# Kernel tuning notes

Hardware: AMD Instinct MI355X
Metric: run time of the kernel (lower is better)

## Reference

```python
import jax, jax.numpy as jnp
import numpy as np

B, S, D = 4, 2048, 512
DT_RANK, N = 32, 16  # dt_rank, d_state
EPS = 1e-5


def setup_inputs() -> dict:
    key = jax.random.key(0)
    ks = jax.random.split(key, 8)
    def w(k, shape, scale):
        return jax.random.normal(k, shape, dtype=jnp.float32) * scale
    return {
        "x": w(ks[0], (B, S, D), 1.0),
        "gamma": jnp.ones((D,), jnp.float32),
        "beta": jnp.zeros((D,), jnp.float32),
        "W_proj": w(ks[1], (D, D), D ** -0.5),
        "b_proj": jnp.zeros((D,), jnp.float32),
        "W_fwd": w(ks[2], (D, D), D ** -0.5),
        "b_fwd": jnp.zeros((D,), jnp.float32),
        "W_bwd": w(ks[3], (D, D), D ** -0.5),
        "b_bwd": jnp.zeros((D,), jnp.float32),
        "W_dbc": w(ks[4], (D, DT_RANK + 2 * N), D ** -0.5),
        "W_dt": w(ks[5], (DT_RANK, D), DT_RANK ** -0.5),
        "b_dt": jnp.zeros((D,), jnp.float32),
        "A_log": jnp.log(jnp.tile(jnp.arange(1, N + 1, dtype=jnp.float32), (D, 1))),
        "D_ssm": jnp.ones((D,), jnp.float32),
    }


def _ssm(x, A_log, D_ssm, W_dbc, W_dt, b_dt):
    # x: (B, S, D) with D == dim_inner
    A = -jnp.exp(A_log)                                   # (D, N)
    dbc = x @ W_dbc                                       # (B, S, dt_rank + 2N)
    delta = jax.nn.softplus(dbc[..., :DT_RANK] @ W_dt + b_dt)  # (B, S, D)
    Bm = dbc[..., DT_RANK:DT_RANK + N]                    # (B, S, N)
    Cm = dbc[..., DT_RANK + N:]                           # (B, S, N)
    deltaA = jnp.exp(delta[..., None] * A)                # (B, S, D, N)
    BX = (delta * x)[..., None] * Bm[:, :, None, :]       # (B, S, D, N)
    def combine(c1, c2):
        a1, b1 = c1
        a2, b2 = c2
        return a1 * a2, a2 * b1 + b2
    _, hs = jax.lax.associative_scan(combine, (deltaA, BX), axis=1)
    y = jnp.einsum('bsdn,bsn->bsd', hs, Cm) + D_ssm * x
    return y


def reference(x, gamma, beta, W_proj, b_proj, W_fwd, b_fwd, W_bwd, b_bwd,
              W_dbc, W_dt, b_dt, A_log, D_ssm):
    skip = x
    mu = jnp.mean(x, axis=-1, keepdims=True)
    var = jnp.var(x, axis=-1, keepdims=True)
    xn = (x - mu) * jax.lax.rsqrt(var + EPS) * gamma + beta
    z1 = xn @ W_proj + b_proj
    x1 = z1  # source applies the SAME self.proj twice -> identical outputs
    # kernel-size-1 conv1d == pointwise linear over channels
    fwd = x1 @ W_fwd + b_fwd
    x1_ssm = _ssm(fwd, A_log, D_ssm, W_dbc, W_dt, b_dt)  # computed but unused in source (dead code)
    bwd = x1 @ W_bwd + bb if False else x1 @ W_bwd + b_bwd
    x2 = _ssm(bwd, A_log, D_ssm, W_dbc, W_dt, b_dt)
    z = jax.nn.silu(z1)
    return x1 * z + x2 * z + skip
```

## Files before the change

kernel.cpp:

```cpp
#include <hip/hip_runtime.h>
#include <hip/hip_bf16.h>
#include <math.h>

#define Bb 4
#define Sdim 2048
#define Ddim 512
#define Nn16 16
#define TOK 8192
#define NCh 64
#define LCh 32

using bf16x8 = __attribute__((ext_vector_type(8))) __bf16;
using f32x4  = __attribute__((ext_vector_type(4))) float;

__device__ __forceinline__ unsigned short f2bf(float f) {
    unsigned int u = __float_as_uint(f);
    u += 0x7fffu + ((u >> 16) & 1u);
    return (unsigned short)(u >> 16);
}
__device__ __forceinline__ float bf2f(unsigned short h) {
    return __uint_as_float(((unsigned int)h) << 16);
}

#define GLD16(g, l) __builtin_amdgcn_global_load_lds( \
    (const __attribute__((address_space(1))) void*)(g), \
    (__attribute__((address_space(3))) void*)(l), 16, 0, 0)

__device__ __forceinline__ float softplus_f(float v) {
    return v > 20.f ? v : log1pf(__expf(v));
}

__global__ __launch_bounds__(256) void prep_all(
    const float* __restrict__ x, const float* __restrict__ gamma, const float* __restrict__ beta,
    const float* __restrict__ Wp, const float* __restrict__ Wb,
    const float* __restrict__ Wdbc, const float* __restrict__ Wdt,
    ushort* __restrict__ xn, ushort* __restrict__ Wpt, ushort* __restrict__ Wbt,
    ushort* __restrict__ Wdbct, ushort* __restrict__ WdtT)
{
    int blk = blockIdx.x;
    int tid = threadIdx.x;
    if (blk < 560) {
        __shared__ float tb[32 * 33];
        int xx = tid & 31, yy0 = tid >> 5;
        const float* in; ushort* outT; int K, N, bx, by;
        if (blk < 256)      { in = Wp;   outT = Wpt;   K = 512; N = 512; bx = (blk & 15) * 32; by = (blk >> 4) * 32; }
        else if (blk < 512) { int t = blk - 256; in = Wb; outT = Wbt; K = 512; N = 512; bx = (t & 15) * 32; by = (t >> 4) * 32; }
        else if (blk < 544) { int t = blk - 512; in = Wdbc; outT = Wdbct; K = 512; N = 64; bx = (t & 1) * 32; by = (t >> 1) * 32; }
        else                { int t = blk - 544; in = Wdt; outT = WdtT; K = 32; N = 512; bx = t * 32; by = 0; }
        #pragma unroll
        for (int yy = yy0; yy < 32; yy += 8)
            tb[yy * 33 + xx] = in[(size_t)(by + yy) * N + bx + xx];
        __syncthreads();
        #pragma unroll
        for (int yy = yy0; yy < 32; yy += 8)
            outT[(size_t)(bx + yy) * K + by + xx] = f2bf(tb[xx * 33 + yy]);
    } else {
        int bid = blk - 560;
        int w = tid >> 6, lane = tid & 63;
        const float4* g4 = (const float4*)gamma;
        const float4* b4 = (const float4*)beta;
        float4 g0 = g4[lane], g1 = g4[lane + 64];
        float4 be0 = b4[lane], be1 = b4[lane + 64];
        for (int rr = 0; rr < 8; ++rr) {
            int row = bid * 32 + w * 8 + rr;
            const float4* xr = (const float4*)(x + (size_t)row * Ddim);
            float4 v0 = xr[lane];
            float4 v1 = xr[lane + 64];
            float s = v0.x + v0.y + v0.z + v0.w + v1.x + v1.y + v1.z + v1.w;
            float q = v0.x*v0.x + v0.y*v0.y + v0.z*v0.z + v0.w*v0.w
                    + v1.x*v1.x + v1.y*v1.y + v1.z*v1.z + v1.w*v1.w;
            #pragma unroll
            for (int m = 1; m <= 32; m <<= 1) { s += __shfl_xor(s, m); q += __shfl_xor(q, m); }
            float mu = s * (1.0f / Ddim);
            float var = q * (1.0f / Ddim) - mu * mu;
            float rs = rsqrtf(var + 1e-5f);
            ushort4 u0, u1;
            u0.x = f2bf((v0.x - mu) * rs * g0.x + be0.x);
            u0.y = f2bf((v0.y - mu) * rs * g0.y + be0.y);
            u0.z = f2bf((v0.z - mu) * rs * g0.z + be0.z);
            u0.w = f2bf((v0.w - mu) * rs * g0.w + be0.w);
            u1.x = f2bf((v1.x - mu) * rs * g1.x + be1.x);
            u1.y = f2bf((v1.y - mu) * rs * g1.y + be1.y);
            u1.z = f2bf((v1.z - mu) * rs * g1.z + be1.z);
            u1.w = f2bf((v1.w - mu) * rs * g1.w + be1.w);
            *(ushort4*)(xn + (size_t)row * Ddim + lane * 4) = u0;
            *(ushort4*)(xn + (size_t)row * Ddim + 256 + lane * 4) = u1;
        }
    }
}

__global__ __launch_bounds__(256) void gemm64(
    const ushort* __restrict__ A,
    const ushort* __restrict__ Bt,
    const float* __restrict__ bias,
    ushort* __restrict__ Cb)
{
    __shared__ __align__(16) ushort As[64 * 64];
    __shared__ __align__(16) ushort Bs[64 * 64];
    int tid = threadIdx.x, w = tid >> 6, lane = tid & 63;
    int bm = blockIdx.x * 64, bn = blockIdx.y * 64;
    int quad = lane >> 4, l16 = lane & 15;
    int srow8 = lane >> 3;
    int scolx = ((lane & 7) ^ srow8) * 8;
    int cof0 = (quad ^ (l16 & 7)) * 8;
    int cof1 = ((4 + quad) ^ (l16 & 7)) * 8;
    f32x4 acc[4] = {};

    for (int k0 = 0; k0 < 512; k0 += 64) {
        __syncthreads();
        #pragma unroll
        for (int s = 0; s < 2; ++s) {
            int r = w * 16 + s * 8;
            GLD16(A  + (size_t)(bm + r + srow8) * 512 + k0 + scolx, &As[r * 64]);
            GLD16(Bt + (size_t)(bn + r + srow8) * 512 + k0 + scolx, &Bs[r * 64]);
        }
        __syncthreads();
        #pragma unroll
        for (int ks = 0; ks < 2; ++ks) {
            int cof = ks ? cof1 : cof0;
            bf16x8 bfr = *(const bf16x8*)(const void*)&Bs[(w * 16 + l16) * 64 + cof];
            #pragma unroll
            for (int i = 0; i < 4; ++i) {
                bf16x8 af = *(const bf16x8*)(const void*)&As[(16 * i + l16) * 64 + cof];
                acc[i] = __builtin_amdgcn_mfma_f32_16x16x32_bf16(af, bfr, acc[i], 0, 0, 0);
            }
        }
    }
    int col = bn + w * 16 + l16;
    float bv = bias[col];
    #pragma unroll
    for (int i = 0; i < 4; ++i) {
        int row = bm + 16 * i + quad * 4;
        #pragma unroll
        for (int r = 0; r < 4; ++r)
            Cb[(size_t)(row + r) * 512 + col] = f2bf(acc[i][r] + bv);
    }
}

__global__ __launch_bounds__(256) void dbc_delta(
    const ushort* __restrict__ bwd,
    const ushort* __restrict__ Wdbct,
    const ushort* __restrict__ WdtT,
    const float* __restrict__ b_dt,
    float* __restrict__ BC,
    ushort* __restrict__ delta)
{
    __shared__ __align__(16) ushort As[32 * 64];
    __shared__ __align__(16) ushort Bs[64 * 64];
    __shared__ __align__(16) ushort sdbc[32 * 32];
    int tid = threadIdx.x, w = tid >> 6, lane = tid & 63;
    int bm = blockIdx.x * 32;
    int quad = lane >> 4, l16 = lane & 15;
    int srow8 = lane >> 3;
    int scolx = ((lane & 7) ^ srow8) * 8;
    int cof0 = (quad ^ (l16 & 7)) * 8;
    int cof1 = ((4 + quad) ^ (l16 & 7)) * 8;

    f32x4 acc[2] = {};
    for (int k0 = 0; k0 < 512; k0 += 64) {
        __syncthreads();
        {
            int r = w * 8;
            GLD16(bwd + (size_t)(bm + r + srow8) * 512 + k0 + scolx, &As[r * 64]);
        }
        #pragma unroll
        for (int s = 0; s < 2; ++s) {
            int r = w * 16 + s * 8;
            GLD16(Wdbct + (size_t)(r + srow8) * 512 + k0 + scolx, &Bs[r * 64]);
        }
        __syncthreads();
        #pragma unroll
        for (int ks = 0; ks < 2; ++ks) {
            int cof = ks ? cof1 : cof0;
            bf16x8 bfr = *(const bf16x8*)(const void*)&Bs[(w * 16 + l16) * 64 + cof];
            #pragma unroll
            for (int i = 0; i < 2; ++i) {
                bf16x8 af = *(const bf16x8*)(const void*)&As[(16 * i + l16) * 64 + cof];
                acc[i] = __builtin_amdgcn_mfma_f32_16x16x32_bf16(af, bfr, acc[i], 0, 0, 0);
            }
        }
    }
    {
        int col = w * 16 + l16;
        #pragma unroll
        for (int i = 0; i < 2; ++i) {
            int rl = 16 * i + quad * 4;
            #pragma unroll
            for (int r = 0; r < 4; ++r) {
                float v = acc[i][r];
                if (col < 32) sdbc[(rl + r) * 32 + col] = f2bf(v);
                else          BC[(size_t)(bm + rl + r) * 32 + col - 32] = v;
            }
        }
    }
    __syncthreads();
    bf16x8 af2[2];
    #pragma unroll
    for (int i = 0; i < 2; ++i)
        af2[i] = *(const bf16x8*)(const void*)&sdbc[(16 * i + l16) * 32 + quad * 8];
    int srow16 = lane >> 2, sch = (lane & 3) * 8;
    for (int cn = 0; cn < 4; ++cn) {
        __syncthreads();
        #pragma unroll
        for (int s = 0; s < 2; ++s) {
            int r = w * 32 + s * 16;
            GLD16(WdtT + (size_t)(cn * 128 + r + srow16) * 32 + sch, &Bs[r * 32]);
        }
        __syncthreads();
        #pragma unroll
        for (int j = 0; j < 2; ++j) {
            bf16x8 bfr = *(const bf16x8*)(const void*)&Bs[(w * 32 + j * 16 + l16) * 32 + quad * 8];
            f32x4 a2[2] = {};
            #pragma unroll
            for (int i = 0; i < 2; ++i)
                a2[i] = __builtin_amdgcn_mfma_f32_16x16x32_bf16(af2[i], bfr, a2[i], 0, 0, 0);
            int col = cn * 128 + w * 32 + j * 16 + l16;
            float bv = b_dt[col];
            #pragma unroll
            for (int i = 0; i < 2; ++i) {
                int row = bm + 16 * i + quad * 4;
                #pragma unroll
                for (int r = 0; r < 4; ++r)
                    delta[(size_t)(row + r) * 512 + col] = f2bf(softplus_f(a2[i][r] + bv));
            }
        }
    }
}

__global__ __launch_bounds__(256) void scan_pass1(
    const ushort* __restrict__ delta, const ushort* __restrict__ bwd,
    const float* __restrict__ BC, const float* __restrict__ A_log,
    float* __restrict__ hend, float* __restrict__ sdbuf)
{
    int d = (blockIdx.x << 8) + threadIdx.x;
    int c = blockIdx.y;
    int b = blockIdx.z;

    float A[16];
    {
        const float4* al = (const float4*)(A_log + (size_t)d * 16);
        #pragma unroll
        for (int i = 0; i < 4; ++i) {
            float4 v = al[i];
            A[4*i+0] = -__expf(v.x); A[4*i+1] = -__expf(v.y);
            A[4*i+2] = -__expf(v.z); A[4*i+3] = -__expf(v.w);
        }
    }
    float h[16];
    #pragma unroll
    for (int n = 0; n < 16; ++n) h[n] = 0.f;
    float sd = 0.f;

    size_t base = ((size_t)(b * Sdim + c * LCh)) * Ddim + d;
    const float* bcrow = BC + ((size_t)(b * Sdim + c * LCh)) * 32;

    #pragma unroll 2
    for (int i = 0; i < LCh; ++i) {
        float dlt = bf2f(delta[base + (size_t)i * Ddim]);
        float bw  = bf2f(bwd [base + (size_t)i * Ddim]);
        float4 B0 = *(const float4*)(bcrow + i * 32 + 0);
        float4 B1 = *(const float4*)(bcrow + i * 32 + 4);
        float4 B2 = *(const float4*)(bcrow + i * 32 + 8);
        float4 B3 = *(const float4*)(bcrow + i * 32 + 12);
        sd += dlt;
        float xb = dlt * bw;
        float Bv[16] = {B0.x,B0.y,B0.z,B0.w, B1.x,B1.y,B1.z,B1.w,
                        B2.x,B2.y,B2.z,B2.w, B3.x,B3.y,B3.z,B3.w};
        #pragma unroll
        for (int n = 0; n < 16; ++n)
            h[n] = fmaf(__expf(dlt * A[n]), h[n], xb * Bv[n]);
    }
    size_t cidx = ((((size_t)b * NCh + c) * Ddim) + d) * 16;
    float4* ho = (float4*)(hend + cidx);
    ho[0] = make_float4(h[0],  h[1],  h[2],  h[3]);
    ho[1] = make_float4(h[4],  h[5],  h[6],  h[7]);
    ho[2] = make_float4(h[8],  h[9],  h[10], h[11]);
    ho[3] = make_float4(h[12], h[13], h[14], h[15]);
    sdbuf[((size_t)b * NCh + c) * Ddim + d] = sd;
}

__global__ __launch_bounds__(256) void scan_pass2(
    float* __restrict__ hend, const float* __restrict__ sdbuf,
    const float* __restrict__ A_log)
{
    int gl = blockIdx.x * 256 + threadIdx.x;
    int b = gl >> 13;
    int r = gl & 8191;
    int d = r >> 4;
    float A = -__expf(A_log[r]);
    float hin = 0.f;
    for (int c0 = 0; c0 < NCh; c0 += 8) {
        float he[8], dec[8];
        #pragma unroll
        for (int u = 0; u < 8; ++u) {
            size_t idx = (((size_t)b * NCh + c0 + u) * Ddim) * 16 + r;
            he[u]  = hend[idx];
            dec[u] = __expf(A * sdbuf[((size_t)b * NCh + c0 + u) * Ddim + d]);
        }
        #pragma unroll
        for (int u = 0; u < 8; ++u) {
            size_t idx = (((size_t)b * NCh + c0 + u) * Ddim) * 16 + r;
            hend[idx] = hin;
            hin = fmaf(dec[u], hin, he[u]);
        }
    }
}

__global__ __launch_bounds__(256) void scan_pass3(
    const ushort* __restrict__ delta, const ushort* __restrict__ bwd,
    const float* __restrict__ BC, const ushort* __restrict__ z1,
    const float* __restrict__ x, const float* __restrict__ A_log,
    const float* __restrict__ D_ssm, const float* __restrict__ hin,
    float* __restrict__ out)
{
    int d = (blockIdx.x << 8) + threadIdx.x;
    int c = blockIdx.y;
    int b = blockIdx.z;

    float A[16];
    {
        const float4* al = (const float4*)(A_log + (size_t)d * 16);
        #pragma unroll
        for (int i = 0; i < 4; ++i) {
            float4 v = al[i];
            A[4*i+0] = -__expf(v.x); A[4*i+1] = -__expf(v.y);
            A[4*i+2] = -__expf(v.z); A[4*i+3] = -__expf(v.w);
        }
    }
    float h[16];
    {
        size_t cidx = ((((size_t)b * NCh + c) * Ddim) + d) * 16;
        const float4* hi = (const float4*)(hin + cidx);
        float4 h0 = hi[0], h1 = hi[1], h2 = hi[2], h3 = hi[3];
        h[0]=h0.x; h[1]=h0.y; h[2]=h0.z; h[3]=h0.w;
        h[4]=h1.x; h[5]=h1.y; h[6]=h1.z; h[7]=h1.w;
        h[8]=h2.x; h[9]=h2.y; h[10]=h2.z; h[11]=h2.w;
        h[12]=h3.x; h[13]=h3.y; h[14]=h3.z; h[15]=h3.w;
    }
    float Dd = D_ssm[d];

    size_t base = ((size_t)(b * Sdim + c * LCh)) * Ddim + d;
    const float* bcrow = BC + ((size_t)(b * Sdim + c * LCh)) * 32;

    #pragma unroll 2
    for (int i = 0; i < LCh; ++i) {
        float dlt = bf2f(delta[base + (size_t)i * Ddim]);
        float bw  = bf2f(bwd [base + (size_t)i * Ddim]);
        float z1v = bf2f(z1  [base + (size_t)i * Ddim]);
        float xv  = x[base + (size_t)i * Ddim];
        float4 B0 = *(const float4*)(bcrow + i * 32 + 0);
        float4 B1 = *(const float4*)(bcrow + i * 32 + 4);
        float4 B2 = *(const float4*)(bcrow + i * 32 + 8);
        float4 B3 = *(const float4*)(bcrow + i * 32 + 12);
        float4 C0 = *(const float4*)(bcrow + i * 32 + 16);
        float4 C1 = *(const float4*)(bcrow + i * 32 + 20);
        float4 C2 = *(const float4*)(bcrow + i * 32 + 24);
        float4 C3 = *(const float4*)(bcrow + i * 32 + 28);
        float Bv[16] = {B0.x,B0.y,B0.z,B0.w, B1.x,B1.y,B1.z,B1.w,
                        B2.x,B2.y,B2.z,B2.w, B3.x,B3.y,B3.z,B3.w};
        float Cv[16] = {C0.x,C0.y,C0.z,C0.w, C1.x,C1.y,C1.z,C1.w,
                        C2.x,C2.y,C2.z,C2.w, C3.x,C3.y,C3.z,C3.w};
        float xb = dlt * bw;
        float y  = Dd * bw;
        #pragma unroll
        for (int n = 0; n < 16; ++n) {
            h[n] = fmaf(__expf(dlt * A[n]), h[n], xb * Bv[n]);
            y = fmaf(h[n], Cv[n], y);
        }
        float silu = z1v / (1.f + __expf(-z1v));
        out[base + (size_t)i * Ddim] = fmaf(z1v + y, silu, xv);
    }
}

extern "C" void kernel_launch(void* const* d_in, const int* in_sizes, int n_in,
                              void* d_out, int out_size, void* d_ws, size_t ws_size,
                              hipStream_t stream) {
    const float* x      = (const float*)d_in[0];
    const float* gamma  = (const float*)d_in[1];
    const float* beta   = (const float*)d_in[2];
    const float* W_proj = (const float*)d_in[3];
    const float* b_proj = (const float*)d_in[4];
    const float* W_bwd  = (const float*)d_in[7];
    const float* b_bwd  = (const float*)d_in[8];
    const float* W_dbc  = (const float*)d_in[9];
    const float* W_dt   = (const float*)d_in[10];
    const float* b_dt   = (const float*)d_in[11];
    const float* A_log  = (const float*)d_in[12];
    const float* D_ssm  = (const float*)d_in[13];
    float* out = (float*)d_out;

    char* p = (char*)d_ws;
    ushort* xn_bf    = (ushort*)p;
    ushort* z1_bf    = (ushort*)(p + (8ull  << 20));
    ushort* bwd_bf   = (ushort*)(p + (16ull << 20));
    ushort* delta_bf = (ushort*)(p + (24ull << 20));
    float*  BC       = (float*) (p + (33ull << 20));
    float*  hend     = (float*) (p + (34ull << 20));
    float*  sdbuf    = (float*) (p + (42ull << 20));
    ushort* Wpt      = (ushort*)(p + (43ull << 20));
    ushort* Wbt      = Wpt   + (size_t)512 * 512;
    ushort* Wdbct    = Wbt   + (size_t)512 * 512;
    ushort* WdtT     = Wdbct + (size_t)64 * 512;

    prep_all<<<dim3(816), dim3(256), 0, stream>>>(
        x, gamma, beta, W_proj, W_bwd, W_dbc, W_dt, xn_bf, Wpt, Wbt, Wdbct, WdtT);
    gemm64<<<dim3(128, 8), dim3(256), 0, stream>>>(xn_bf, Wpt, b_proj, z1_bf);
    gemm64<<<dim3(128, 8), dim3(256), 0, stream>>>(z1_bf, Wbt, b_bwd, bwd_bf);
    dbc_delta<<<dim3(256), dim3(256), 0, stream>>>(bwd_bf, Wdbct, WdtT, b_dt, BC, delta_bf);
    scan_pass1<<<dim3(2, NCh, Bb), dim3(256), 0, stream>>>(delta_bf, bwd_bf, BC, A_log, hend, sdbuf);
    scan_pass2<<<dim3(128), dim3(256), 0, stream>>>(hend, sdbuf, A_log);
    scan_pass3<<<dim3(2, NCh, Bb), dim3(256), 0, stream>>>(delta_bf, bwd_bf, BC, z1_bf, x, A_log, D_ssm, hend, out);
}
```

Measured before the change: 191.9 us.

## Fuse all stages into one cooperative persistent kernel with grid syncs

Replaces the seven separate kernel launches with a single cooperative kernel of 256 blocks that loops over the work items of each stage and separates the stages with grid-wide syncs. This is meant to remove per-launch overhead and inter-kernel gaps. The trade-off is one block per CU and fewer waves in flight for the memory-bound scan and GEMM stages. The multi-kernel path is kept as a fallback if the cooperative launch fails.

```diff
diff --git a/kernel.cpp b/kernel.cpp
--- a/kernel.cpp
+++ b/kernel.cpp
@@ -1,6 +1,9 @@
 #include <hip/hip_runtime.h>
+#include <hip/hip_cooperative_groups.h>
 #include <hip/hip_bf16.h>
 #include <math.h>
+
+namespace cg = cooperative_groups;
 
 #define Bb 4
 #define Sdim 2048
@@ -30,23 +33,21 @@
     return v > 20.f ? v : log1pf(__expf(v));
 }
 
-__global__ __launch_bounds__(256) void prep_all(
-    const float* __restrict__ x, const float* __restrict__ gamma, const float* __restrict__ beta,
-    const float* __restrict__ Wp, const float* __restrict__ Wb,
-    const float* __restrict__ Wdbc, const float* __restrict__ Wdt,
-    ushort* __restrict__ xn, ushort* __restrict__ Wpt, ushort* __restrict__ Wbt,
-    ushort* __restrict__ Wdbct, ushort* __restrict__ WdtT)
-{
-    int blk = blockIdx.x;
-    int tid = threadIdx.x;
-    if (blk < 560) {
-        __shared__ float tb[32 * 33];
+
+__device__ __forceinline__ void prep_job(
+    int job, int tid, char* smem,
+    const float* x, const float* gamma, const float* beta,
+    const float* Wp, const float* Wb, const float* Wdbc, const float* Wdt,
+    ushort* xn, ushort* Wpt, ushort* Wbt, ushort* Wdbct, ushort* WdtT)
+{
+    if (job < 560) {
+        float* tb = (float*)smem;
         int xx = tid & 31, yy0 = tid >> 5;
         const float* in; ushort* outT; int K, N, bx, by;
-        if (blk < 256)      { in = Wp;   outT = Wpt;   K = 512; N = 512; bx = (blk & 15) * 32; by = (blk >> 4) * 32; }
-        else if (blk < 512) { int t = blk - 256; in = Wb; outT = Wbt; K = 512; N = 512; bx = (t & 15) * 32; by = (t >> 4) * 32; }
-        else if (blk < 544) { int t = blk - 512; in = Wdbc; outT = Wdbct; K = 512; N = 64; bx = (t & 1) * 32; by = (t >> 1) * 32; }
-        else                { int t = blk - 544; in = Wdt; outT = WdtT; K = 32; N = 512; bx = t * 32; by = 0; }
+        if (job < 256)      { in = Wp;   outT = Wpt;   K = 512; N = 512; bx = (job & 15) * 32; by = (job >> 4) * 32; }
+        else if (job < 512) { int t = job - 256; in = Wb; outT = Wbt; K = 512; N = 512; bx = (t & 15) * 32; by = (t >> 4) * 32; }
+        else if (job < 544) { int t = job - 512; in = Wdbc; outT = Wdbct; K = 512; N = 64; bx = (t & 1) * 32; by = (t >> 1) * 32; }
+        else                { int t = job - 544; in = Wdt; outT = WdtT; K = 32; N = 512; bx = t * 32; by = 0; }
         #pragma unroll
         for (int yy = yy0; yy < 32; yy += 8)
             tb[yy * 33 + xx] = in[(size_t)(by + yy) * N + bx + xx];
@@ -55,7 +56,7 @@
         for (int yy = yy0; yy < 32; yy += 8)
             outT[(size_t)(bx + yy) * K + by + xx] = f2bf(tb[xx * 33 + yy]);
     } else {
-        int bid = blk - 560;
+        int bid = job - 560;
         int w = tid >> 6, lane = tid & 63;
         const float4* g4 = (const float4*)gamma;
         const float4* b4 = (const float4*)beta;
@@ -89,16 +90,13 @@
     }
 }
 
-__global__ __launch_bounds__(256) void gemm64(
-    const ushort* __restrict__ A,
-    const ushort* __restrict__ Bt,
-    const float* __restrict__ bias,
-    ushort* __restrict__ Cb)
-{
-    __shared__ __align__(16) ushort As[64 * 64];
-    __shared__ __align__(16) ushort Bs[64 * 64];
+__device__ __forceinline__ void gemm64_tile(
+    const ushort* A, const ushort* Bt, const float* bias, ushort* Cb,
+    int bm, int bn, char* smem)
+{
+    ushort* As = (ushort*)smem;
+    ushort* Bs = (ushort*)(smem + 8192);
     int tid = threadIdx.x, w = tid >> 6, lane = tid & 63;
-    int bm = blockIdx.x * 64, bn = blockIdx.y * 64;
     int quad = lane >> 4, l16 = lane & 15;
     int srow8 = lane >> 3;
     int scolx = ((lane & 7) ^ srow8) * 8;
@@ -135,21 +133,17 @@
         for (int r = 0; r < 4; ++r)
             Cb[(size_t)(row + r) * 512 + col] = f2bf(acc[i][r] + bv);
     }
-}
-
-__global__ __launch_bounds__(256) void dbc_delta(
-    const ushort* __restrict__ bwd,
-    const ushort* __restrict__ Wdbct,
-    const ushort* __restrict__ WdtT,
-    const float* __restrict__ b_dt,
-    float* __restrict__ BC,
-    ushort* __restrict__ delta)
-{
-    __shared__ __align__(16) ushort As[32 * 64];
-    __shared__ __align__(16) ushort Bs[64 * 64];
-    __shared__ __align__(16) ushort sdbc[32 * 32];
+    __syncthreads();
+}
+
+__device__ __forceinline__ void dbc_delta_tile(
+    const ushort* bwd, const ushort* Wdbct, const ushort* WdtT,
+    const float* b_dt, float* BC, ushort* delta, int bm, char* smem)
+{
+    ushort* As   = (ushort*)smem;
+    ushort* Bs   = (ushort*)(smem + 4096);
+    ushort* sdbc = (ushort*)(smem + 12288);
     int tid = threadIdx.x, w = tid >> 6, lane = tid & 63;
-    int bm = blockIdx.x * 32;
     int quad = lane >> 4, l16 = lane & 15;
     int srow8 = lane >> 3;
     int scolx = ((lane & 7) ^ srow8) * 8;
@@ -225,17 +219,14 @@
             }
         }
     }
-}
-
-__global__ __launch_bounds__(256) void scan_pass1(
-    const ushort* __restrict__ delta, const ushort* __restrict__ bwd,
-    const float* __restrict__ BC, const float* __restrict__ A_log,
-    float* __restrict__ hend, float* __restrict__ sdbuf)
-{
-    int d = (blockIdx.x << 8) + threadIdx.x;
-    int c = blockIdx.y;
-    int b = blockIdx.z;
-
+    __syncthreads();
+}
+
+__device__ __forceinline__ void scan1_job(
+    int d, int c, int b,
+    const ushort* delta, const ushort* bwd, const float* BC,
+    const float* A_log, float* hend, float* sdbuf)
+{
     float A[16];
     {
         const float4* al = (const float4*)(A_log + (size_t)d * 16);
@@ -250,10 +241,8 @@
     #pragma unroll
     for (int n = 0; n < 16; ++n) h[n] = 0.f;
     float sd = 0.f;
-
     size_t base = ((size_t)(b * Sdim + c * LCh)) * Ddim + d;
     const float* bcrow = BC + ((size_t)(b * Sdim + c * LCh)) * 32;
-
     #pragma unroll 2
     for (int i = 0; i < LCh; ++i) {
         float dlt = bf2f(delta[base + (size_t)i * Ddim]);
@@ -279,11 +268,9 @@
     sdbuf[((size_t)b * NCh + c) * Ddim + d] = sd;
 }
 
-__global__ __launch_bounds__(256) void scan_pass2(
-    float* __restrict__ hend, const float* __restrict__ sdbuf,
-    const float* __restrict__ A_log)
-{
-    int gl = blockIdx.x * 256 + threadIdx.x;
+__device__ __forceinline__ void scan2_job(
+    int gl, float* hend, const float* sdbuf, const float* A_log)
+{
     int b = gl >> 13;
     int r = gl & 8191;
     int d = r >> 4;
@@ -306,17 +293,12 @@
     }
 }
 
-__global__ __launch_bounds__(256) void scan_pass3(
-    const ushort* __restrict__ delta, const ushort* __restrict__ bwd,
-    const float* __restrict__ BC, const ushort* __restrict__ z1,
-    const float* __restrict__ x, const float* __restrict__ A_log,
-    const float* __restrict__ D_ssm, const float* __restrict__ hin,
-    float* __restrict__ out)
-{
-    int d = (blockIdx.x << 8) + threadIdx.x;
-    int c = blockIdx.y;
-    int b = blockIdx.z;
-
+__device__ __forceinline__ void scan3_job(
+    int d, int c, int b,
+    const ushort* delta, const ushort* bwd, const float* BC, const ushort* z1,
+    const float* x, const float* A_log, const float* D_ssm,
+    const float* hin, float* out)
+{
     float A[16];
     {
         const float4* al = (const float4*)(A_log + (size_t)d * 16);
@@ -338,10 +320,8 @@
         h[12]=h3.x; h[13]=h3.y; h[14]=h3.z; h[15]=h3.w;
     }
     float Dd = D_ssm[d];
-
     size_t base = ((size_t)(b * Sdim + c * LCh)) * Ddim + d;
     const float* bcrow = BC + ((size_t)(b * Sdim + c * LCh)) * 32;
-
     #pragma unroll 2
     for (int i = 0; i < LCh; ++i) {
         float dlt = bf2f(delta[base + (size_t)i * Ddim]);
@@ -372,42 +352,163 @@
     }
 }
 
+struct FP {
+    const float *x, *gamma, *beta, *Wp, *Wb, *Wdbc, *Wdt, *bp, *bb, *bdt, *A_log, *D_ssm;
+    ushort *xn, *Wpt, *Wbt, *Wdbct, *WdtT, *z1, *bwd, *delta;
+    float *BC, *hend, *sdbuf, *out;
+};
+
+__global__ __launch_bounds__(256) void fused(FP P) {
+    cg::grid_group g = cg::this_grid();
+    __shared__ __align__(16) char smem[16384];
+    int blk = blockIdx.x;
+    int tid = threadIdx.x;
+
+    #pragma unroll 1
+    for (int it = 0; it < 4; ++it) {
+        int job = it * 256 + blk;
+        if (job < 816)
+            prep_job(job, tid, smem, P.x, P.gamma, P.beta, P.Wp, P.Wb, P.Wdbc, P.Wdt,
+                     P.xn, P.Wpt, P.Wbt, P.Wdbct, P.WdtT);
+        __syncthreads();
+    }
+    g.sync();
+    #pragma unroll 1
+    for (int it = 0; it < 4; ++it) {
+        int job = it * 256 + blk;
+        gemm64_tile(P.xn, P.Wpt, P.bp, P.z1, (job & 127) * 64, (job >> 7) * 64, smem);
+    }
+    g.sync();
+    #pragma unroll 1
+    for (int it = 0; it < 4; ++it) {
+        int job = it * 256 + blk;
+        gemm64_tile(P.z1, P.Wbt, P.bb, P.bwd, (job & 127) * 64, (job >> 7) * 64, smem);
+    }
+    g.sync();
+    dbc_delta_tile(P.bwd, P.Wdbct, P.WdtT, P.bdt, P.BC, P.delta, blk * 32, smem);
+    g.sync();
+    #pragma unroll 1
+    for (int it = 0; it < 2; ++it) {
+        int job = it * 256 + blk;
+        int d = ((job & 1) << 8) + tid;
+        int c = (job >> 1) & 63;
+        int b = job >> 7;
+        scan1_job(d, c, b, P.delta, P.bwd, P.BC, P.A_log, P.hend, P.sdbuf);
+    }
+    g.sync();
+    if (blk < 128)
+        scan2_job(blk * 256 + tid, P.hend, P.sdbuf, P.A_log);
+    g.sync();
+    #pragma unroll 1
+    for (int it = 0; it < 2; ++it) {
+        int job = it * 256 + blk;
+        int d = ((job & 1) << 8) + tid;
+        int c = (job >> 1) & 63;
+        int b = job >> 7;
+        scan3_job(d, c, b, P.delta, P.bwd, P.BC, P.z1, P.x, P.A_log, P.D_ssm, P.hend, P.out);
+    }
+}
+
+__global__ __launch_bounds__(256) void prep_all_k(
+    const float* __restrict__ x, const float* __restrict__ gamma, const float* __restrict__ beta,
+    const float* __restrict__ Wp, const float* __restrict__ Wb,
+    const float* __restrict__ Wdbc, const float* __restrict__ Wdt,
+    ushort* __restrict__ xn, ushort* __restrict__ Wpt, ushort* __restrict__ Wbt,
+    ushort* __restrict__ Wdbct, ushort* __restrict__ WdtT)
+{
+    __shared__ __align__(16) char smem[4352];
+    prep_job(blockIdx.x, threadIdx.x, smem, x, gamma, beta, Wp, Wb, Wdbc, Wdt,
+             xn, Wpt, Wbt, Wdbct, WdtT);
+}
+
+__global__ __launch_bounds__(256) void gemm64_k(
+    const ushort* __restrict__ A, const ushort* __restrict__ Bt,
+    const float* __restrict__ bias, ushort* __restrict__ Cb)
+{
+    __shared__ __align__(16) char smem[16384];
+    gemm64_tile(A, Bt, bias, Cb, blockIdx.x * 64, blockIdx.y * 64, smem);
+}
+
+__global__ __launch_bounds__(256) void dbc_delta_k(
+    const ushort* __restrict__ bwd, const ushort* __restrict__ Wdbct,
+    const ushort* __restrict__ WdtT, const float* __restrict__ b_dt,
+    float* __restrict__ BC, ushort* __restrict__ delta)
+{
+    __shared__ __align__(16) char smem[16384];
+    dbc_delta_tile(bwd, Wdbct, WdtT, b_dt, BC, delta, blockIdx.x * 32, smem);
+}
+
+__global__ __launch_bounds__(256) void scan_pass1_k(
+    const ushort* __restrict__ delta, const ushort* __restrict__ bwd,
+    const float* __restrict__ BC, const float* __restrict__ A_log,
+    float* __restrict__ hend, float* __restrict__ sdbuf)
+{
+    scan1_job((blockIdx.x << 8) + threadIdx.x, blockIdx.y, blockIdx.z,
+              delta, bwd, BC, A_log, hend, sdbuf);
+}
+
+__global__ __launch_bounds__(256) void scan_pass2_k(
+    float* __restrict__ hend, const float* __restrict__ sdbuf,
+    const float* __restrict__ A_log)
+{
+    scan2_job(blockIdx.x * 256 + threadIdx.x, hend, sdbuf, A_log);
+}
+
+__global__ __launch_bounds__(256) void scan_pass3_k(
+    const ushort* __restrict__ delta, const ushort* __restrict__ bwd,
+    const float* __restrict__ BC, const ushort* __restrict__ z1,
+    const float* __restrict__ x, const float* __restrict__ A_log,
+    const float* __restrict__ D_ssm, const float* __restrict__ hin,
+    float* __restrict__ out)
+{
+    scan3_job((blockIdx.x << 8) + threadIdx.x, blockIdx.y, blockIdx.z,
+              delta, bwd, BC, z1, x, A_log, D_ssm, hin, out);
+}
+
 extern "C" void kernel_launch(void* const* d_in, const int* in_sizes, int n_in,
                               void* d_out, int out_size, void* d_ws, size_t ws_size,
                               hipStream_t stream) {
-    const float* x      = (const float*)d_in[0];
-    const float* gamma  = (const float*)d_in[1];
-    const float* beta   = (const float*)d_in[2];
-    const float* W_proj = (const float*)d_in[3];
-    const float* b_proj = (const float*)d_in[4];
-    const float* W_bwd  = (const float*)d_in[7];
-    const float* b_bwd  = (const float*)d_in[8];
-    const float* W_dbc  = (const float*)d_in[9];
-    const float* W_dt   = (const float*)d_in[10];
-    const float* b_dt   = (const float*)d_in[11];
-    const float* A_log  = (const float*)d_in[12];
-    const float* D_ssm  = (const float*)d_in[13];
-    float* out = (float*)d_out;
-
     char* p = (char*)d_ws;
-    ushort* xn_bf    = (ushort*)p;
-    ushort* z1_bf    = (ushort*)(p + (8ull  << 20));
-    ushort* bwd_bf   = (ushort*)(p + (16ull << 20));
-    ushort* delta_bf = (ushort*)(p + (24ull << 20));
-    float*  BC       = (float*) (p + (33ull << 20));
-    float*  hend     = (float*) (p + (34ull << 20));
-    float*  sdbuf    = (float*) (p + (42ull << 20));
-    ushort* Wpt      = (ushort*)(p + (43ull << 20));
-    ushort* Wbt      = Wpt   + (size_t)512 * 512;
-    ushort* Wdbct    = Wbt   + (size_t)512 * 512;
-    ushort* WdtT     = Wdbct + (size_t)64 * 512;
-
-    prep_all<<<dim3(816), dim3(256), 0, stream>>>(
-        x, gamma, beta, W_proj, W_bwd, W_dbc, W_dt, xn_bf, Wpt, Wbt, Wdbct, WdtT);
-    gemm64<<<dim3(128, 8), dim3(256), 0, stream>>>(xn_bf, Wpt, b_proj, z1_bf);
-    gemm64<<<dim3(128, 8), dim3(256), 0, stream>>>(z1_bf, Wbt, b_bwd, bwd_bf);
-    dbc_delta<<<dim3(256), dim3(256), 0, stream>>>(bwd_bf, Wdbct, WdtT, b_dt, BC, delta_bf);
-    scan_pass1<<<dim3(2, NCh, Bb), dim3(256), 0, stream>>>(delta_bf, bwd_bf, BC, A_log, hend, sdbuf);
-    scan_pass2<<<dim3(128), dim3(256), 0, stream>>>(hend, sdbuf, A_log);
-    scan_pass3<<<dim3(2, NCh, Bb), dim3(256), 0, stream>>>(delta_bf, bwd_bf, BC, z1_bf, x, A_log, D_ssm, hend, out);
-}
+    FP P;
+    P.x     = (const float*)d_in[0];
+    P.gamma = (const float*)d_in[1];
+    P.beta  = (const float*)d_in[2];
+    P.Wp    = (const float*)d_in[3];
+    P.bp    = (const float*)d_in[4];
+    P.Wb    = (const float*)d_in[7];
+    P.bb    = (const float*)d_in[8];
+    P.Wdbc  = (const float*)d_in[9];
+    P.Wdt   = (const float*)d_in[10];
+    P.bdt   = (const float*)d_in[11];
+    P.A_log = (const float*)d_in[12];
+    P.D_ssm = (const float*)d_in[13];
+    P.out   = (float*)d_out;
+
+    P.xn    = (ushort*)p;
+    P.z1    = (ushort*)(p + (8ull  << 20));
+    P.bwd   = (ushort*)(p + (16ull << 20));
+    P.delta = (ushort*)(p + (24ull << 20));
+    P.BC    = (float*) (p + (33ull << 20));
+    P.hend  = (float*) (p + (34ull << 20));
+    P.sdbuf = (float*) (p + (42ull << 20));
+    P.Wpt   = (ushort*)(p + (43ull << 20));
+    P.Wbt   = P.Wpt   + (size_t)512 * 512;
+    P.Wdbct = P.Wbt   + (size_t)512 * 512;
+    P.WdtT  = P.Wdbct + (size_t)64 * 512;
+
+    void* args[] = { &P };
+    hipError_t rc = hipLaunchCooperativeKernel((void*)fused, dim3(256), dim3(256),
+                                               args, 0, stream);
+    if (rc != hipSuccess) {
+        (void)hipGetLastError();
+        prep_all_k<<<dim3(816), dim3(256), 0, stream>>>(
+            P.x, P.gamma, P.beta, P.Wp, P.Wb, P.Wdbc, P.Wdt,
+            P.xn, P.Wpt, P.Wbt, P.Wdbct, P.WdtT);
+        gemm64_k<<<dim3(128, 8), dim3(256), 0, stream>>>(P.xn, P.Wpt, P.bp, P.z1);
+        gemm64_k<<<dim3(128, 8), dim3(256), 0, stream>>>(P.z1, P.Wbt, P.bb, P.bwd);
+        dbc_delta_k<<<dim3(256), dim3(256), 0, stream>>>(P.bwd, P.Wdbct, P.WdtT, P.bdt, P.BC, P.delta);
+        scan_pass1_k<<<dim3(2, NCh, Bb), dim3(256), 0, stream>>>(P.delta, P.bwd, P.BC, P.A_log, P.hend, P.sdbuf);
+        scan_pass2_k<<<dim3(128), dim3(256), 0, stream>>>(P.hend, P.sdbuf, P.A_log);
+        scan_pass3_k<<<dim3(2, NCh, Bb), dim3(256), 0, stream>>>(P.delta, P.bwd, P.BC, P.z1, P.x, P.A_log, P.D_ssm, P.hend, P.out);
+    }
+}
```

Result: slower. 463.6 us (+141.5%).
